# Optimization experiments

Hardware: AMD Instinct MI355X
Metric: run time of the kernel (lower is better)

Reference implementation:

```python
import jax, jax.numpy as jnp
import numpy as np

D = 512
H = 8
DH = D // H


def setup_inputs() -> dict:
    key = jax.random.key(0)
    ks = jax.random.split(key, 6)
    B, S = 2, 4096
    scale = 1.0 / np.sqrt(D)
    x = jax.random.normal(ks[0], (B, S, D), dtype=jnp.float32)
    W_q = jax.random.normal(ks[1], (D, D), dtype=jnp.float32) * scale
    W_k = jax.random.normal(ks[2], (D, D), dtype=jnp.float32) * scale
    W_v = jax.random.normal(ks[3], (D, D), dtype=jnp.float32) * scale
    W_proj = jax.random.normal(ks[4], (D, D), dtype=jnp.float32) * scale
    b_proj = jax.random.normal(ks[5], (D,), dtype=jnp.float32) * 0.01
    return {"x": x, "W_q": W_q, "W_k": W_k, "W_v": W_v,
            "W_proj": W_proj, "b_proj": b_proj}


def reference(x, W_q, W_k, W_v, W_proj, b_proj):
    B, S, _ = x.shape
    # torch Linear: y = x @ W.T
    def proj(W):
        y = jnp.einsum('bsd,ed->bse', x, W)
        return y.reshape(B, S, H, DH).transpose(0, 2, 1, 3)  # [B,H,S,DH]
    q, k, v = proj(W_q), proj(W_k), proj(W_v)
    scores = jnp.einsum('bhqd,bhkd->bhqk', q, k) / np.sqrt(DH)  # [B,H,S,S]
    causal = jnp.tril(jnp.ones((S, S), dtype=bool))
    neg = jnp.finfo(scores.dtype).min
    scores = jnp.where(causal[None, None, :, :], scores, neg)
    w = jax.nn.softmax(scores, axis=-1)
    attn = jnp.einsum('bhqk,bhkd->bhqd', w, v)  # [B,H,S,DH]
    attn = attn.transpose(0, 2, 1, 3).reshape(B, S, D)
    return jnp.einsum('bsd,ed->bse', attn, W_proj) + b_proj
```

## Files before the change

kernel.cpp:

```cpp
#include <hip/hip_runtime.h>
#include <hip/hip_bf16.h>
#include <stdint.h>

#define D_MODEL 512
#define NH 8
#define DH 64
#define SEQ 4096
#define NBH 16
#define NX  (2 * SEQ * D_MODEL)
#define NW  (D_MODEL * D_MODEL)

typedef __attribute__((ext_vector_type(8))) short bf16x8;
typedef __attribute__((ext_vector_type(4))) float f32x4;
typedef __attribute__((ext_vector_type(16))) float f32x16;

#define CSCALE 0.18033688011112042f

__device__ __forceinline__ uint32_t pkbf(float a, float b) {
    uint32_t r;
    asm("v_cvt_pk_bf16_f32 %0, %1, %2" : "=v"(r) : "v"(a), "v"(b));
    return r;
}

#define SWZ(R) (((R) + ((R) >> 2)) & 3)

#define BAR() do {                                          \
    asm volatile("s_waitcnt lgkmcnt(0)" ::: "memory");      \
    __builtin_amdgcn_s_barrier();                           \
} while (0)

__device__ __forceinline__ bf16x8 cvt8(float4 u, float4 v, float s) {
    union { uint32_t w[4]; bf16x8 h; } r;
    r.w[0] = pkbf(u.x * s, u.y * s); r.w[1] = pkbf(u.z * s, u.w * s);
    r.w[2] = pkbf(v.x * s, v.y * s); r.w[3] = pkbf(v.z * s, v.w * s);
    return r.h;
}

__global__ __launch_bounds__(256) void cvt_pre(
    const float* __restrict__ x,
    const float* __restrict__ Wq, const float* __restrict__ Wk,
    const float* __restrict__ Wv, const float* __restrict__ Wp,
    short* __restrict__ xb, short* __restrict__ Wb)
{
    const size_t t = ((size_t)blockIdx.x * 256 + threadIdx.x) * 8;
    const float* src; short* dst; float s = 1.0f; size_t off;
    if (t < NX) {
        src = x; dst = xb; off = t;
    } else {
        const size_t u = t - NX;
        const int w = (int)(u >> 18);
        off = u & (NW - 1);
        src = (w == 0) ? Wq : (w == 1) ? Wk : (w == 2) ? Wv : Wp;
        dst = Wb + ((size_t)w << 18);
        s = (w == 0) ? CSCALE : 1.0f;
    }
    float4 a = *(const float4*)(src + off);
    float4 b = *(const float4*)(src + off + 4);
    *(bf16x8*)(dst + off) = cvt8(a, b, s);
}

__global__ __launch_bounds__(256) void qkv_kernel(
    const short* __restrict__ xb, const short* __restrict__ Wb,
    short* __restrict__ Qb, short* __restrict__ Kb, short* __restrict__ Vt)
{
    __shared__ __align__(16) short at[2][4096];
    __shared__ __align__(16) short bt[2][4096];

    const int tid  = threadIdx.x;
    const int wave = tid >> 6;
    const int lane = tid & 63;
    const int ln = lane & 15, quad = lane >> 4;
    const int z = blockIdx.z;
    const short* W = Wb + ((size_t)z << 18);
    const int m0 = blockIdx.x * 128;
    const int n0 = blockIdx.y * 128;
    const int mh = (wave & 1) * 64, nh = (wave >> 1) * 64;

    const int ck0 = tid, ck1 = tid + 256;
    const int R0 = ck0 >> 2, R1 = ck1 >> 2;
    const int c0 = (ck0 & 3) ^ SWZ(R0), c1 = (ck1 & 3) ^ SWZ(R1);

    bf16x8 ra0, ra1, rb0, rb1;
    auto loadAB = [&](int kc) {
        ra0 = *(const bf16x8*)(xb + (size_t)(m0 + R0) * D_MODEL + kc + c0 * 8);
        ra1 = *(const bf16x8*)(xb + (size_t)(m0 + R1) * D_MODEL + kc + c1 * 8);
        rb0 = *(const bf16x8*)(W + (size_t)(n0 + R0) * D_MODEL + kc + c0 * 8);
        rb1 = *(const bf16x8*)(W + (size_t)(n0 + R1) * D_MODEL + kc + c1 * 8);
    };
    auto writeAB = [&](int buf) {
        *(bf16x8*)&at[buf][ck0 * 8] = ra0;
        *(bf16x8*)&at[buf][ck1 * 8] = ra1;
        *(bf16x8*)&bt[buf][ck0 * 8] = rb0;
        *(bf16x8*)&bt[buf][ck1 * 8] = rb1;
    };

    f32x4 acc[4][4] = {};

    loadAB(0);
    writeAB(0);

    for (int s = 0; s < 16; ++s) {
        const int cur = s & 1;
        BAR();
        if (s < 15) loadAB((s + 1) * 32);

        bf16x8 a[4], b[4];
#pragma unroll
        for (int i = 0; i < 4; ++i) {
            const int R = mh + i * 16 + ln;
            a[i] = *(const bf16x8*)(&at[cur][R * 32 + ((quad ^ SWZ(R)) * 8)]);
        }
#pragma unroll
        for (int j = 0; j < 4; ++j) {
            const int R = nh + j * 16 + ln;
            b[j] = *(const bf16x8*)(&bt[cur][R * 32 + ((quad ^ SWZ(R)) * 8)]);
        }
        __builtin_amdgcn_s_setprio(1);
#pragma unroll
        for (int i = 0; i < 4; ++i)
#pragma unroll
            for (int j = 0; j < 4; ++j)
                acc[i][j] = __builtin_amdgcn_mfma_f32_16x16x32_bf16(
                    a[i], b[j], acc[i][j], 0, 0, 0);
        __builtin_amdgcn_s_setprio(0);

        if (s < 15) writeAB(cur ^ 1);
    }

    if (z == 2) {
#pragma unroll
        for (int i = 0; i < 4; ++i) {
            const int row0 = m0 + mh + i * 16 + quad * 4;
            const int bb = row0 >> 12, sq = row0 & (SEQ - 1);
#pragma unroll
            for (int j = 0; j < 4; ++j) {
                const int n = n0 + nh + j * 16 + ln;
                const int h = n >> 6, dh = n & 63;
                uint2 st;
                st.x = pkbf(acc[i][j][0], acc[i][j][1]);
                st.y = pkbf(acc[i][j][2], acc[i][j][3]);
                *(uint2*)(Vt + (size_t)((bb * NH + h) * DH + dh) * SEQ + sq) = st;
            }
        }
    } else {
        short* P = (z == 0) ? Qb : Kb;
#pragma unroll
        for (int i = 0; i < 4; ++i)
#pragma unroll
            for (int j = 0; j < 4; ++j) {
                const int n = n0 + nh + j * 16 + ln;
                const int h = n >> 6, dh = n & 63;
                const uint32_t lo = pkbf(acc[i][j][0], acc[i][j][1]);
                const uint32_t hi2 = pkbf(acc[i][j][2], acc[i][j][3]);
#pragma unroll
                for (int r = 0; r < 4; ++r) {
                    const int row = m0 + mh + i * 16 + quad * 4 + r;
                    const int bb = row >> 12, sq = row & (SEQ - 1);
                    const uint32_t w = (r < 2) ? lo : hi2;
                    P[((size_t)((bb * NH + h) * SEQ + sq) << 6) + dh] =
                        (short)((r & 1) ? (w >> 16) : (w & 0xffff));
                }
            }
    }
}

__global__ __launch_bounds__(256) void attn_kernel(
    const short* __restrict__ Qb, const short* __restrict__ Kb,
    const short* __restrict__ Vt, short* __restrict__ ao)
{
    __shared__ __align__(16) short kt[2][4096];
    __shared__ __align__(16) short vt[2][4096];

    const int tid  = threadIdx.x;
    const int wave = tid >> 6;
    const int lane = tid & 63;
    const int l31 = lane & 31, hi = lane >> 5;
    const int bh = blockIdx.y;
    const int w_ = (blockIdx.x + 4 * bh) & 31;
    const int g2 = ((bh >> 3) & 1) ? (31 - w_) : w_;
    const short* Qp = Qb + (size_t)bh * SEQ * DH;
    const short* Kp = Kb + (size_t)bh * SEQ * DH;
    const short* Vp = Vt + (size_t)bh * DH * SEQ;
    const int bb = bh >> 3, h = bh & 7;
    const int q0 = g2 * 128 + wave * 32;
    const int myq = q0 + l31;
    const int jdiag = q0 >> 6;
    const int jmax = 2 * g2 + 1;

    const int ckA = tid, ckB = tid + 256;
    const int RA = ckA >> 3, RB = ckB >> 3;
    const int cA = (ckA & 7) ^ (RA & 7), cB = (ckB & 7) ^ (RB & 7);
    const int RA31 = RA & 31, RB31 = RB & 31;
    const int kkA = (RA & 32) + ((RA31 & 8) << 1) + ((RA31 & 4) << 1)
                  + ((RA31 & 16) >> 2) + (RA31 & 3);
    const int kkB = (RB & 32) + ((RB31 & 8) << 1) + ((RB31 & 4) << 1)
                  + ((RB31 & 16) >> 2) + (RB31 & 3);
    const size_t kOffA = ((size_t)kkA << 6) + cA * 8;
    const size_t kOffB = ((size_t)kkB << 6) + cB * 8;
    const size_t vOffA = (size_t)RA * SEQ + cA * 8;
    const size_t vOffB = (size_t)RB * SEQ + cB * 8;

    bf16x8 sk0, sk1, sv0, sv1;
    auto load_tile = [&](int j) {
        const size_t k0 = (size_t)j * 64;
        sk0 = *(const bf16x8*)(Kp + (k0 << 6) + kOffA);
        sk1 = *(const bf16x8*)(Kp + (k0 << 6) + kOffB);
        sv0 = *(const bf16x8*)(Vp + vOffA + k0);
        sv1 = *(const bf16x8*)(Vp + vOffB + k0);
    };
    auto write_tile = [&](int buf) {
        *(bf16x8*)&kt[buf][ckA * 8] = sk0;
        *(bf16x8*)&kt[buf][ckB * 8] = sk1;
        *(bf16x8*)&vt[buf][ckA * 8] = sv0;
        *(bf16x8*)&vt[buf][ckB * 8] = sv1;
    };

    bf16x8 qf[4];
#pragma unroll
    for (int c = 0; c < 4; ++c)
        qf[c] = *(const bf16x8*)(Qp + (size_t)myq * DH + c * 16 + hi * 8);

    const bf16x8 ones = { (short)0x3F80, (short)0x3F80, (short)0x3F80,
                          (short)0x3F80, (short)0x3F80, (short)0x3F80,
                          (short)0x3F80, (short)0x3F80 };

    f32x16 o0 = {}, o1 = {};
    f32x16 lacc = {};

    load_tile(0);
    write_tile(0);
    load_tile(1);
    BAR();

    for (int j = 0; j <= jmax; ++j) {
        const int cur = j & 1;
        if (j < jmax) {
            write_tile(cur ^ 1);
            if (j + 1 < jmax) load_tile(j + 2);
        }

        if ((j << 6) <= q0 + 31) {
            f32x16 s0 = {}, s1 = {};
            const int sw = l31 & 7;
            __builtin_amdgcn_s_setprio(1);
#pragma unroll
            for (int c = 0; c < 4; ++c) {
                const int pc = ((2 * c + hi) ^ sw) * 8;
                bf16x8 a0 = *(const bf16x8*)(&kt[cur][l31 * 64 + pc]);
                bf16x8 a1 = *(const bf16x8*)(&kt[cur][(32 + l31) * 64 + pc]);
                s0 = __builtin_amdgcn_mfma_f32_32x32x16_bf16(a0, qf[c], s0, 0, 0, 0);
                s1 = __builtin_amdgcn_mfma_f32_32x32x16_bf16(a1, qf[c], s1, 0, 0, 0);
            }
            __builtin_amdgcn_s_setprio(0);
            if (j >= jdiag) {
                const int k0 = j * 64;
#pragma unroll
                for (int reg = 0; reg < 16; ++reg) {
                    const int kl = ((reg >> 2) & 1) * 16 + hi * 8
                                 + ((reg >> 3) & 1) * 4 + (reg & 3);
                    if (k0 + kl > myq)      s0[reg] = -3e38f;
                    if (k0 + 32 + kl > myq) s1[reg] = -3e38f;
                }
            }
#pragma unroll
            for (int i = 0; i < 16; ++i) {
                s0[i] = __builtin_amdgcn_exp2f(s0[i]);
                s1[i] = __builtin_amdgcn_exp2f(s1[i]);
            }

            union { uint32_t u[4]; bf16x8 v; } p00, p01, p10, p11;
            p00.u[0] = pkbf(s0[0], s0[1]);   p00.u[1] = pkbf(s0[2], s0[3]);
            p00.u[2] = pkbf(s0[8], s0[9]);   p00.u[3] = pkbf(s0[10], s0[11]);
            p01.u[0] = pkbf(s0[4], s0[5]);   p01.u[1] = pkbf(s0[6], s0[7]);
            p01.u[2] = pkbf(s0[12], s0[13]); p01.u[3] = pkbf(s0[14], s0[15]);
            p10.u[0] = pkbf(s1[0], s1[1]);   p10.u[1] = pkbf(s1[2], s1[3]);
            p10.u[2] = pkbf(s1[8], s1[9]);   p10.u[3] = pkbf(s1[10], s1[11]);
            p11.u[0] = pkbf(s1[4], s1[5]);   p11.u[1] = pkbf(s1[6], s1[7]);
            p11.u[2] = pkbf(s1[12], s1[13]); p11.u[3] = pkbf(s1[14], s1[15]);

            __builtin_amdgcn_s_setprio(1);
            lacc = __builtin_amdgcn_mfma_f32_32x32x16_bf16(ones, p00.v, lacc, 0, 0, 0);
            lacc = __builtin_amdgcn_mfma_f32_32x32x16_bf16(ones, p01.v, lacc, 0, 0, 0);
            lacc = __builtin_amdgcn_mfma_f32_32x32x16_bf16(ones, p10.v, lacc, 0, 0, 0);
            lacc = __builtin_amdgcn_mfma_f32_32x32x16_bf16(ones, p11.v, lacc, 0, 0, 0);

            {
                const short* vrow = &vt[cur][l31 * 64];
                bf16x8 v00 = *(const bf16x8*)(vrow + (((0 + hi) ^ sw) * 8));
                bf16x8 v01 = *(const bf16x8*)(vrow + (((2 + hi) ^ sw) * 8));
                bf16x8 v10 = *(const bf16x8*)(vrow + (((4 + hi) ^ sw) * 8));
                bf16x8 v11 = *(const bf16x8*)(vrow + (((6 + hi) ^ sw) * 8));
                o0 = __builtin_amdgcn_mfma_f32_32x32x16_bf16(v00, p00.v, o0, 0, 0, 0);
                o0 = __builtin_amdgcn_mfma_f32_32x32x16_bf16(v01, p01.v, o0, 0, 0, 0);
                o0 = __builtin_amdgcn_mfma_f32_32x32x16_bf16(v10, p10.v, o0, 0, 0, 0);
                o0 = __builtin_amdgcn_mfma_f32_32x32x16_bf16(v11, p11.v, o0, 0, 0, 0);
            }
            {
                const short* vrow = &vt[cur][(32 + l31) * 64];
                bf16x8 v00 = *(const bf16x8*)(vrow + (((0 + hi) ^ sw) * 8));
                bf16x8 v01 = *(const bf16x8*)(vrow + (((2 + hi) ^ sw) * 8));
                bf16x8 v10 = *(const bf16x8*)(vrow + (((4 + hi) ^ sw) * 8));
                bf16x8 v11 = *(const bf16x8*)(vrow + (((6 + hi) ^ sw) * 8));
                o1 = __builtin_amdgcn_mfma_f32_32x32x16_bf16(v00, p00.v, o1, 0, 0, 0);
                o1 = __builtin_amdgcn_mfma_f32_32x32x16_bf16(v01, p01.v, o1, 0, 0, 0);
                o1 = __builtin_amdgcn_mfma_f32_32x32x16_bf16(v10, p10.v, o1, 0, 0, 0);
                o1 = __builtin_amdgcn_mfma_f32_32x32x16_bf16(v11, p11.v, o1, 0, 0, 0);
            }
            __builtin_amdgcn_s_setprio(0);
        }
        BAR();
    }
    const float inv = 1.0f / lacc[0];
    short* orow = ao + (size_t)(bb * SEQ + myq) * D_MODEL + h * DH;
#pragma unroll
    for (int c = 0; c < 4; ++c) {
        uint2 st;
        st.x = pkbf(o0[4 * c] * inv,     o0[4 * c + 1] * inv);
        st.y = pkbf(o0[4 * c + 2] * inv, o0[4 * c + 3] * inv);
        *(uint2*)(orow + 8 * c + 4 * hi) = st;
    }
#pragma unroll
    for (int c = 0; c < 4; ++c) {
        uint2 st;
        st.x = pkbf(o1[4 * c] * inv,     o1[4 * c + 1] * inv);
        st.y = pkbf(o1[4 * c + 2] * inv, o1[4 * c + 3] * inv);
        *(uint2*)(orow + 32 + 8 * c + 4 * hi) = st;
    }
}

__global__ __launch_bounds__(256) void proj_kernel(
    const short* __restrict__ attn, const short* __restrict__ Wpb,
    const float* __restrict__ bias, float* __restrict__ out)
{
    __shared__ __align__(16) short at[2][2048];
    __shared__ __align__(16) short bt[2][4096];

    const int tid  = threadIdx.x;
    const int wave = tid >> 6;
    const int lane = tid & 63;
    const int ln = lane & 15, quad = lane >> 4;
    const int m0 = blockIdx.x * 64;
    const int n0 = blockIdx.y * 128;
    const int mh = (wave & 1) * 32, nh = (wave >> 1) * 64;

    const int RA = tid >> 2, cAc = (tid & 3) ^ SWZ(RA);
    const int ck0 = tid, ck1 = tid + 256;
    const int R0 = ck0 >> 2, R1 = ck1 >> 2;
    const int c0 = (ck0 & 3) ^ SWZ(R0), c1 = (ck1 & 3) ^ SWZ(R1);

    bf16x8 raA, rb0, rb1;
    auto loadAB = [&](int kc) {
        raA = *(const bf16x8*)(attn + (size_t)(m0 + RA) * D_MODEL + kc + cAc * 8);
        rb0 = *(const bf16x8*)(Wpb + (size_t)(n0 + R0) * D_MODEL + kc + c0 * 8);
        rb1 = *(const bf16x8*)(Wpb + (size_t)(n0 + R1) * D_MODEL + kc + c1 * 8);
    };
    auto writeAB = [&](int buf) {
        *(bf16x8*)&at[buf][tid * 8] = raA;
        *(bf16x8*)&bt[buf][ck0 * 8] = rb0;
        *(bf16x8*)&bt[buf][ck1 * 8] = rb1;
    };

    f32x4 acc[2][4] = {};

    loadAB(0);
    writeAB(0);

    for (int s = 0; s < 16; ++s) {
        const int cur = s & 1;
        BAR();
        if (s < 15) loadAB((s + 1) * 32);

        bf16x8 a[2], b[4];
#pragma unroll
        for (int i = 0; i < 2; ++i) {
            const int R = mh + i * 16 + ln;
            a[i] = *(const bf16x8*)(&at[cur][R * 32 + ((quad ^ SWZ(R)) * 8)]);
        }
#pragma unroll
        for (int j = 0; j < 4; ++j) {
            const int R = nh + j * 16 + ln;
            b[j] = *(const bf16x8*)(&bt[cur][R * 32 + ((quad ^ SWZ(R)) * 8)]);
        }
        __builtin_amdgcn_s_setprio(1);
#pragma unroll
        for (int i = 0; i < 2; ++i)
#pragma unroll
            for (int j = 0; j < 4; ++j)
                acc[i][j] = __builtin_amdgcn_mfma_f32_16x16x32_bf16(
                    a[i], b[j], acc[i][j], 0, 0, 0);
        __builtin_amdgcn_s_setprio(0);

        if (s < 15) writeAB(cur ^ 1);
    }
#pragma unroll
    for (int j = 0; j < 4; ++j) {
        const int n = n0 + nh + j * 16 + ln;
        const float bv = bias[n];
#pragma unroll
        for (int i = 0; i < 2; ++i)
#pragma unroll
            for (int r = 0; r < 4; ++r) {
                const int row = m0 + mh + i * 16 + quad * 4 + r;
                out[(size_t)row * D_MODEL + n] = acc[i][j][r] + bv;
            }
    }
}

extern "C" void kernel_launch(void* const* d_in, const int* in_sizes, int n_in,
                              void* d_out, int out_size, void* d_ws, size_t ws_size,
                              hipStream_t stream) {
    const float* x  = (const float*)d_in[0];
    const float* Wq = (const float*)d_in[1];
    const float* Wk = (const float*)d_in[2];
    const float* Wv = (const float*)d_in[3];
    const float* Wp = (const float*)d_in[4];
    const float* bp = (const float*)d_in[5];
    float* out = (float*)d_out;

    short* Qb = (short*)d_ws;
    short* Kb = Qb + (size_t)NBH * SEQ * DH;
    short* Vt = Kb + (size_t)NBH * SEQ * DH;
    short* ab = Vt + (size_t)NBH * SEQ * DH;
    short* Wb = ab + (size_t)NBH * SEQ * DH;

    short* xb = (short*)d_out;

    cvt_pre<<<dim3((NX + 4 * NW) / (8 * 256)), 256, 0, stream>>>(
        x, Wq, Wk, Wv, Wp, xb, Wb);
    qkv_kernel<<<dim3(64, 4, 3), 256, 0, stream>>>(xb, Wb, Qb, Kb, Vt);
    attn_kernel<<<dim3(32, NBH), 256, 0, stream>>>(Qb, Kb, Vt, ab);
    proj_kernel<<<dim3(128, 4), 256, 0, stream>>>(ab, Wb + 3 * (size_t)NW, bp, out);
}
```

Measured before the change: 169.4 us.

## Halve attention block size to 64 queries and remap grid for XCD locality

The attention kernel now uses 128-thread blocks covering 64 queries each, launched as a 1D grid of 1024 blocks instead of 32x16 blocks of 256 threads. Block ids are remapped so each XCD handles two batch-heads, and query chunks are interleaved from both ends of the causal triangle to balance load. Each thread now loads four K/V chunks per tile instead of two, and the per-wave skip of fully masked tiles is removed because every tile up to the diagonal is needed by both waves. The intent is more parallelism, better L2 locality per XCD, and less idle tail work. The cost is that each block reloads K/V tiles for fewer queries, which doubles total K/V traffic into shared memory.

```diff
diff --git a/kernel.cpp b/kernel.cpp
--- a/kernel.cpp
+++ b/kernel.cpp
@@ -164,7 +164,7 @@
     }
 }
 
-__global__ __launch_bounds__(256) void attn_kernel(
+__global__ __launch_bounds__(128) void attn_kernel(
     const short* __restrict__ Qb, const short* __restrict__ Kb,
     const short* __restrict__ Vt, short* __restrict__ ao)
 {
@@ -175,44 +175,52 @@
     const int wave = tid >> 6;
     const int lane = tid & 63;
     const int l31 = lane & 31, hi = lane >> 5;
-    const int bh = blockIdx.y;
-    const int w_ = (blockIdx.x + 4 * bh) & 31;
-    const int g2 = ((bh >> 3) & 1) ? (31 - w_) : w_;
+
+    const int bid = blockIdx.x;
+    const int xcd = bid & 7;
+    const int kk_ = bid >> 3;
+    const int bh  = 2 * xcd + (kk_ & 1);
+    const int ci  = kk_ >> 1;
+    const int chunk = (ci & 1) ? (63 - (ci >> 1)) : (ci >> 1);
+
     const short* Qp = Qb + (size_t)bh * SEQ * DH;
     const short* Kp = Kb + (size_t)bh * SEQ * DH;
     const short* Vp = Vt + (size_t)bh * DH * SEQ;
     const int bb = bh >> 3, h = bh & 7;
-    const int q0 = g2 * 128 + wave * 32;
+    const int q0 = chunk * 64 + wave * 32;
     const int myq = q0 + l31;
-    const int jdiag = q0 >> 6;
-    const int jmax = 2 * g2 + 1;
-
-    const int ckA = tid, ckB = tid + 256;
-    const int RA = ckA >> 3, RB = ckB >> 3;
-    const int cA = (ckA & 7) ^ (RA & 7), cB = (ckB & 7) ^ (RB & 7);
-    const int RA31 = RA & 31, RB31 = RB & 31;
-    const int kkA = (RA & 32) + ((RA31 & 8) << 1) + ((RA31 & 4) << 1)
-                  + ((RA31 & 16) >> 2) + (RA31 & 3);
-    const int kkB = (RB & 32) + ((RB31 & 8) << 1) + ((RB31 & 4) << 1)
-                  + ((RB31 & 16) >> 2) + (RB31 & 3);
-    const size_t kOffA = ((size_t)kkA << 6) + cA * 8;
-    const size_t kOffB = ((size_t)kkB << 6) + cB * 8;
-    const size_t vOffA = (size_t)RA * SEQ + cA * 8;
-    const size_t vOffB = (size_t)RB * SEQ + cB * 8;
-
-    bf16x8 sk0, sk1, sv0, sv1;
+    const int jdiag = chunk;
+    const int jmax = chunk;
+
+    int ckv[4]; size_t kOff[4], vOff[4];
+#pragma unroll
+    for (int p = 0; p < 4; ++p) {
+        const int ck = tid + 128 * p;
+        const int R = ck >> 3;
+        const int cc = (ck & 7) ^ (R & 7);
+        const int R31 = R & 31;
+        const int kp = (R & 32) + ((R31 & 8) << 1) + ((R31 & 4) << 1)
+                     + ((R31 & 16) >> 2) + (R31 & 3);
+        ckv[p] = ck;
+        kOff[p] = ((size_t)kp << 6) + cc * 8;
+        vOff[p] = (size_t)R * SEQ + cc * 8;
+    }
+
+    bf16x8 sk[4], sv[4];
     auto load_tile = [&](int j) {
         const size_t k0 = (size_t)j * 64;
-        sk0 = *(const bf16x8*)(Kp + (k0 << 6) + kOffA);
-        sk1 = *(const bf16x8*)(Kp + (k0 << 6) + kOffB);
-        sv0 = *(const bf16x8*)(Vp + vOffA + k0);
-        sv1 = *(const bf16x8*)(Vp + vOffB + k0);
+#pragma unroll
+        for (int p = 0; p < 4; ++p) {
+            sk[p] = *(const bf16x8*)(Kp + (k0 << 6) + kOff[p]);
+            sv[p] = *(const bf16x8*)(Vp + vOff[p] + k0);
+        }
     };
     auto write_tile = [&](int buf) {
-        *(bf16x8*)&kt[buf][ckA * 8] = sk0;
-        *(bf16x8*)&kt[buf][ckB * 8] = sk1;
-        *(bf16x8*)&vt[buf][ckA * 8] = sv0;
-        *(bf16x8*)&vt[buf][ckB * 8] = sv1;
+#pragma unroll
+        for (int p = 0; p < 4; ++p) {
+            *(bf16x8*)&kt[buf][ckv[p] * 8] = sk[p];
+            *(bf16x8*)&vt[buf][ckv[p] * 8] = sv[p];
+        }
     };
 
     bf16x8 qf[4];
@@ -239,75 +247,73 @@
             if (j + 1 < jmax) load_tile(j + 2);
         }
 
-        if ((j << 6) <= q0 + 31) {
-            f32x16 s0 = {}, s1 = {};
-            const int sw = l31 & 7;
-            __builtin_amdgcn_s_setprio(1);
-#pragma unroll
-            for (int c = 0; c < 4; ++c) {
-                const int pc = ((2 * c + hi) ^ sw) * 8;
-                bf16x8 a0 = *(const bf16x8*)(&kt[cur][l31 * 64 + pc]);
-                bf16x8 a1 = *(const bf16x8*)(&kt[cur][(32 + l31) * 64 + pc]);
-                s0 = __builtin_amdgcn_mfma_f32_32x32x16_bf16(a0, qf[c], s0, 0, 0, 0);
-                s1 = __builtin_amdgcn_mfma_f32_32x32x16_bf16(a1, qf[c], s1, 0, 0, 0);
+        f32x16 s0 = {}, s1 = {};
+        const int sw = l31 & 7;
+        __builtin_amdgcn_s_setprio(1);
+#pragma unroll
+        for (int c = 0; c < 4; ++c) {
+            const int pc = ((2 * c + hi) ^ sw) * 8;
+            bf16x8 a0 = *(const bf16x8*)(&kt[cur][l31 * 64 + pc]);
+            bf16x8 a1 = *(const bf16x8*)(&kt[cur][(32 + l31) * 64 + pc]);
+            s0 = __builtin_amdgcn_mfma_f32_32x32x16_bf16(a0, qf[c], s0, 0, 0, 0);
+            s1 = __builtin_amdgcn_mfma_f32_32x32x16_bf16(a1, qf[c], s1, 0, 0, 0);
+        }
+        __builtin_amdgcn_s_setprio(0);
+        if (j >= jdiag) {
+            const int k0 = j * 64;
+#pragma unroll
+            for (int reg = 0; reg < 16; ++reg) {
+                const int kl = ((reg >> 2) & 1) * 16 + hi * 8
+                             + ((reg >> 3) & 1) * 4 + (reg & 3);
+                if (k0 + kl > myq)      s0[reg] = -3e38f;
+                if (k0 + 32 + kl > myq) s1[reg] = -3e38f;
             }
-            __builtin_amdgcn_s_setprio(0);
-            if (j >= jdiag) {
-                const int k0 = j * 64;
-#pragma unroll
-                for (int reg = 0; reg < 16; ++reg) {
-                    const int kl = ((reg >> 2) & 1) * 16 + hi * 8
-                                 + ((reg >> 3) & 1) * 4 + (reg & 3);
-                    if (k0 + kl > myq)      s0[reg] = -3e38f;
-                    if (k0 + 32 + kl > myq) s1[reg] = -3e38f;
-                }
-            }
-#pragma unroll
-            for (int i = 0; i < 16; ++i) {
-                s0[i] = __builtin_amdgcn_exp2f(s0[i]);
-                s1[i] = __builtin_amdgcn_exp2f(s1[i]);
-            }
-
-            union { uint32_t u[4]; bf16x8 v; } p00, p01, p10, p11;
-            p00.u[0] = pkbf(s0[0], s0[1]);   p00.u[1] = pkbf(s0[2], s0[3]);
-            p00.u[2] = pkbf(s0[8], s0[9]);   p00.u[3] = pkbf(s0[10], s0[11]);
-            p01.u[0] = pkbf(s0[4], s0[5]);   p01.u[1] = pkbf(s0[6], s0[7]);
-            p01.u[2] = pkbf(s0[12], s0[13]); p01.u[3] = pkbf(s0[14], s0[15]);
-            p10.u[0] = pkbf(s1[0], s1[1]);   p10.u[1] = pkbf(s1[2], s1[3]);
-            p10.u[2] = pkbf(s1[8], s1[9]);   p10.u[3] = pkbf(s1[10], s1[11]);
-            p11.u[0] = pkbf(s1[4], s1[5]);   p11.u[1] = pkbf(s1[6], s1[7]);
-            p11.u[2] = pkbf(s1[12], s1[13]); p11.u[3] = pkbf(s1[14], s1[15]);
-
-            __builtin_amdgcn_s_setprio(1);
-            lacc = __builtin_amdgcn_mfma_f32_32x32x16_bf16(ones, p00.v, lacc, 0, 0, 0);
-            lacc = __builtin_amdgcn_mfma_f32_32x32x16_bf16(ones, p01.v, lacc, 0, 0, 0);
-            lacc = __builtin_amdgcn_mfma_f32_32x32x16_bf16(ones, p10.v, lacc, 0, 0, 0);
-            lacc = __builtin_amdgcn_mfma_f32_32x32x16_bf16(ones, p11.v, lacc, 0, 0, 0);
-
-            {
-                const short* vrow = &vt[cur][l31 * 64];
-                bf16x8 v00 = *(const bf16x8*)(vrow + (((0 + hi) ^ sw) * 8));
-                bf16x8 v01 = *(const bf16x8*)(vrow + (((2 + hi) ^ sw) * 8));
-                bf16x8 v10 = *(const bf16x8*)(vrow + (((4 + hi) ^ sw) * 8));
-                bf16x8 v11 = *(const bf16x8*)(vrow + (((6 + hi) ^ sw) * 8));
-                o0 = __builtin_amdgcn_mfma_f32_32x32x16_bf16(v00, p00.v, o0, 0, 0, 0);
-                o0 = __builtin_amdgcn_mfma_f32_32x32x16_bf16(v01, p01.v, o0, 0, 0, 0);
-                o0 = __builtin_amdgcn_mfma_f32_32x32x16_bf16(v10, p10.v, o0, 0, 0, 0);
-                o0 = __builtin_amdgcn_mfma_f32_32x32x16_bf16(v11, p11.v, o0, 0, 0, 0);
-            }
-            {
-                const short* vrow = &vt[cur][(32 + l31) * 64];
-                bf16x8 v00 = *(const bf16x8*)(vrow + (((0 + hi) ^ sw) * 8));
-                bf16x8 v01 = *(const bf16x8*)(vrow + (((2 + hi) ^ sw) * 8));
-                bf16x8 v10 = *(const bf16x8*)(vrow + (((4 + hi) ^ sw) * 8));
-                bf16x8 v11 = *(const bf16x8*)(vrow + (((6 + hi) ^ sw) * 8));
-                o1 = __builtin_amdgcn_mfma_f32_32x32x16_bf16(v00, p00.v, o1, 0, 0, 0);
-                o1 = __builtin_amdgcn_mfma_f32_32x32x16_bf16(v01, p01.v, o1, 0, 0, 0);
-                o1 = __builtin_amdgcn_mfma_f32_32x32x16_bf16(v10, p10.v, o1, 0, 0, 0);
-                o1 = __builtin_amdgcn_mfma_f32_32x32x16_bf16(v11, p11.v, o1, 0, 0, 0);
-            }
-            __builtin_amdgcn_s_setprio(0);
-        }
+        }
+#pragma unroll
+        for (int i = 0; i < 16; ++i) {
+            s0[i] = __builtin_amdgcn_exp2f(s0[i]);
+            s1[i] = __builtin_amdgcn_exp2f(s1[i]);
+        }
+
+        union { uint32_t u[4]; bf16x8 v; } p00, p01, p10, p11;
+        p00.u[0] = pkbf(s0[0], s0[1]);   p00.u[1] = pkbf(s0[2], s0[3]);
+        p00.u[2] = pkbf(s0[8], s0[9]);   p00.u[3] = pkbf(s0[10], s0[11]);
+        p01.u[0] = pkbf(s0[4], s0[5]);   p01.u[1] = pkbf(s0[6], s0[7]);
+        p01.u[2] = pkbf(s0[12], s0[13]); p01.u[3] = pkbf(s0[14], s0[15]);
+        p10.u[0] = pkbf(s1[0], s1[1]);   p10.u[1] = pkbf(s1[2], s1[3]);
+        p10.u[2] = pkbf(s1[8], s1[9]);   p10.u[3] = pkbf(s1[10], s1[11]);
+        p11.u[0] = pkbf(s1[4], s1[5]);   p11.u[1] = pkbf(s1[6], s1[7]);
+        p11.u[2] = pkbf(s1[12], s1[13]); p11.u[3] = pkbf(s1[14], s1[15]);
+
+        __builtin_amdgcn_s_setprio(1);
+        lacc = __builtin_amdgcn_mfma_f32_32x32x16_bf16(ones, p00.v, lacc, 0, 0, 0);
+        lacc = __builtin_amdgcn_mfma_f32_32x32x16_bf16(ones, p01.v, lacc, 0, 0, 0);
+        lacc = __builtin_amdgcn_mfma_f32_32x32x16_bf16(ones, p10.v, lacc, 0, 0, 0);
+        lacc = __builtin_amdgcn_mfma_f32_32x32x16_bf16(ones, p11.v, lacc, 0, 0, 0);
+
+        {
+            const short* vrow = &vt[cur][l31 * 64];
+            bf16x8 v00 = *(const bf16x8*)(vrow + (((0 + hi) ^ sw) * 8));
+            bf16x8 v01 = *(const bf16x8*)(vrow + (((2 + hi) ^ sw) * 8));
+            bf16x8 v10 = *(const bf16x8*)(vrow + (((4 + hi) ^ sw) * 8));
+            bf16x8 v11 = *(const bf16x8*)(vrow + (((6 + hi) ^ sw) * 8));
+            o0 = __builtin_amdgcn_mfma_f32_32x32x16_bf16(v00, p00.v, o0, 0, 0, 0);
+            o0 = __builtin_amdgcn_mfma_f32_32x32x16_bf16(v01, p01.v, o0, 0, 0, 0);
+            o0 = __builtin_amdgcn_mfma_f32_32x32x16_bf16(v10, p10.v, o0, 0, 0, 0);
+            o0 = __builtin_amdgcn_mfma_f32_32x32x16_bf16(v11, p11.v, o0, 0, 0, 0);
+        }
+        {
+            const short* vrow = &vt[cur][(32 + l31) * 64];
+            bf16x8 v00 = *(const bf16x8*)(vrow + (((0 + hi) ^ sw) * 8));
+            bf16x8 v01 = *(const bf16x8*)(vrow + (((2 + hi) ^ sw) * 8));
+            bf16x8 v10 = *(const bf16x8*)(vrow + (((4 + hi) ^ sw) * 8));
+            bf16x8 v11 = *(const bf16x8*)(vrow + (((6 + hi) ^ sw) * 8));
+            o1 = __builtin_amdgcn_mfma_f32_32x32x16_bf16(v00, p00.v, o1, 0, 0, 0);
+            o1 = __builtin_amdgcn_mfma_f32_32x32x16_bf16(v01, p01.v, o1, 0, 0, 0);
+            o1 = __builtin_amdgcn_mfma_f32_32x32x16_bf16(v10, p10.v, o1, 0, 0, 0);
+            o1 = __builtin_amdgcn_mfma_f32_32x32x16_bf16(v11, p11.v, o1, 0, 0, 0);
+        }
+        __builtin_amdgcn_s_setprio(0);
         BAR();
     }
     const float inv = 1.0f / lacc[0];
@@ -428,6 +434,6 @@
     cvt_pre<<<dim3((NX + 4 * NW) / (8 * 256)), 256, 0, stream>>>(
         x, Wq, Wk, Wv, Wp, xb, Wb);
     qkv_kernel<<<dim3(64, 4, 3), 256, 0, stream>>>(xb, Wb, Qb, Kb, Vt);
-    attn_kernel<<<dim3(32, NBH), 256, 0, stream>>>(Qb, Kb, Vt, ab);
+    attn_kernel<<<dim3(1024), 128, 0, stream>>>(Qb, Kb, Vt, ab);
     proj_kernel<<<dim3(128, 4), 256, 0, stream>>>(ab, Wb + 3 * (size_t)NW, bp, out);
 }
```

New measurement: 182.8 us. 7.9% more time.
